# Kernel optimization log

Hardware: AMD Instinct MI355X
Metric: run time of the kernel (lower is better)

The kernel has to match this reference:

```python
import jax, jax.numpy as jnp
import numpy as np

N_GROUP = 64
GROUP_SIZE = 64
INPUT_DIM = 2048
BATCH = 8192
N_MONTN = 512


def setup_inputs() -> dict:
    key = jax.random.key(0)
    k1, k2, k3, k4, k5 = jax.random.split(key, 5)
    x = jax.random.normal(k1, (BATCH, INPUT_DIM), dtype=jnp.float32)
    weight = jax.random.normal(k2, (N_GROUP * GROUP_SIZE, INPUT_DIM), dtype=jnp.float32) * 0.02
    bias = jax.random.normal(k3, (N_GROUP * GROUP_SIZE,), dtype=jnp.float32) * 0.02
    rand_u = jax.random.uniform(k4, (BATCH,), dtype=jnp.float32)
    montn_index = jax.random.randint(k5, (N_MONTN,), 0, INPUT_DIM, dtype=jnp.int32)
    return {"x": x, "weight": weight, "bias": bias, "rand_u": rand_u,
            "montn_index": montn_index}


def reference(x, weight, bias, rand_u, montn_index):
    # Square the weights on monotone input columns (in-place in torch).
    w = weight.at[:, montn_index].set(weight[:, montn_index] ** 2)
    # y = x @ w^T + b  -> [B, n_group * n_group_size]
    y = jnp.einsum('bi,oi->bo', x, w) + bias
    B = y.shape[0]
    # per-group min over contiguous slices, then max over groups
    group_mins = y.reshape(B, N_GROUP, GROUP_SIZE).min(axis=2)  # [B, n_group]
    out = group_mins.max(axis=1)                                 # [B]
    # vectorized Bernoulli: 1.0 if u < sigmoid(out) else 0.0
    sample = (rand_u < jax.nn.sigmoid(out)).astype(jnp.float32)
    return sample.reshape(-1, 1)
```

## Files before the change

### kernel.cpp

```cpp
#include <hip/hip_runtime.h>
#include <cmath>


typedef _Float16 f16x8 __attribute__((ext_vector_type(8)));
typedef float f32x16 __attribute__((ext_vector_type(16)));

#define MARGIN_EPS 4e-3f
#define MAX_UNDEC 96

__device__ __forceinline__ void async_load16(const void* gptr, void* lptr) {
  __builtin_amdgcn_global_load_lds(
      (const __attribute__((address_space(1))) void*)gptr,
      (__attribute__((address_space(3))) void*)lptr, 16, 0, 0);
}

__device__ __forceinline__ float us2f(unsigned short u) {
  return (float)__builtin_bit_cast(_Float16, u);
}

__global__ void convert_split(float* __restrict__ x, float* __restrict__ wgt,
                              const int* __restrict__ montn,
                              int* __restrict__ count) {
  __shared__ unsigned msk[64];
  const int t = threadIdx.x, l = t & 63, w = t >> 6;
  const int r = blockIdx.x * 4 + w;
  const int use_mask = (r >= 8192) ? 1 : 0;
  if (blockIdx.x == 0 && t == 0) *count = 0;
  if (use_mask) {
    if (t < 64) msk[t] = 0u;
    __syncthreads();
    for (int j = t; j < 512; j += 256) {
      const int c = montn[j];
      atomicOr(&msk[c >> 5], 1u << (c & 31));
    }
    __syncthreads();
  }
  float* rowp = use_mask ? (wgt + (size_t)(r - 8192) * 2048)
                         : (x + (size_t)r * 2048);
  float4 v[8];
#pragma unroll
  for (int j = 0; j < 8; ++j) v[j] = ((const float4*)rowp)[l + 64 * j];
  unsigned mw[8];
#pragma unroll
  for (int j = 0; j < 8; ++j)
    mw[j] = use_mask ? msk[(l >> 3) + 8 * j] : 0u;

  unsigned short* up = (unsigned short*)rowp;
#pragma unroll
  for (int j = 0; j < 8; ++j) {
    unsigned short hs[4], ls[4];
    const float* fv = (const float*)&v[j];
#pragma unroll
    for (int c = 0; c < 4; ++c) {
      float f = fv[c];
      if ((mw[j] >> (4 * (l & 7) + c)) & 1u) f = f * f;
      _Float16 h = (_Float16)f;
      float res = f - (float)h;
      _Float16 lo = (_Float16)res;
      hs[c] = __builtin_bit_cast(unsigned short, h);
      ls[c] = __builtin_bit_cast(unsigned short, lo);
    }
    uint2 H, L;
    H.x = (unsigned)hs[0] | ((unsigned)hs[1] << 16);
    H.y = (unsigned)hs[2] | ((unsigned)hs[3] << 16);
    L.x = (unsigned)ls[0] | ((unsigned)ls[1] << 16);
    L.y = (unsigned)ls[2] | ((unsigned)ls[3] << 16);
    *((uint2*)(up + 4 * l + 256 * j)) = H;
    *((uint2*)(up + 2048 + 4 * l + 256 * j)) = L;
  }
}

__global__ __launch_bounds__(256, 4) void gemm_minmax(
    const unsigned short* __restrict__ X, const unsigned short* __restrict__ W,
    const float* __restrict__ bias, float* __restrict__ gmins) {
  __shared__ unsigned short As[128 * 64];
  __shared__ unsigned short Bs[128 * 64];
  const int t = threadIdx.x;
  const int lane = t & 63;
  const int w = t >> 6;
  const int wm = w >> 1, wn = w & 1;
  const int lin = blockIdx.x;
  const int sid = lin >> 3;
  const int m0 = (sid >> 2) * 128;
  const int n0 = ((lin & 7) * 4 + (sid & 3)) * 128;

  const int rowBase = w * 8 + (lane >> 3);
  const int gchunk = ((lane & 7) ^ ((lane >> 3) & 7)) * 8;
  size_t sA[4], sB[4];
#pragma unroll
  for (int c = 0; c < 4; ++c) {
    sA[c] = (size_t)(m0 + c * 32 + rowBase) * 4096 + gchunk;
    sB[c] = (size_t)(n0 + c * 32 + rowBase) * 4096 + gchunk;
  }
  unsigned short* ldsA[4];
  unsigned short* ldsB[4];
#pragma unroll
  for (int c = 0; c < 4; ++c) {
    ldsA[c] = As + c * 2048 + w * 512;
    ldsB[c] = Bs + c * 2048 + w * 512;
  }

  const int l31 = lane & 31, hi32 = lane >> 5;
  int arow[2], brow[2], swz[4];
#pragma unroll
  for (int i = 0; i < 2; ++i) {
    arow[i] = (wm * 64 + i * 32 + l31) * 64;
    brow[i] = (wn * 64 + i * 32 + l31) * 64;
  }
#pragma unroll
  for (int s = 0; s < 4; ++s) swz[s] = ((2 * s + hi32) ^ (lane & 7)) * 8;

  f32x16 acc[2][2];
#pragma unroll
  for (int i = 0; i < 2; ++i)
#pragma unroll
    for (int j = 0; j < 2; ++j) acc[i][j] = (f32x16)(0.f);

#pragma unroll 1
  for (int it = 0; it < 32; ++it) {
    const int kin = it * 64;
    __syncthreads();
#pragma unroll
    for (int c = 0; c < 4; ++c) {
      async_load16(X + sA[c] + kin, ldsA[c]);
      async_load16(W + sB[c] + kin, ldsB[c]);
    }
    __syncthreads();

#pragma unroll
    for (int s = 0; s < 4; ++s) {
      f16x8 a0 = *(const f16x8*)(As + arow[0] + swz[s]);
      f16x8 a1 = *(const f16x8*)(As + arow[1] + swz[s]);
      f16x8 b0 = *(const f16x8*)(Bs + brow[0] + swz[s]);
      f16x8 b1 = *(const f16x8*)(Bs + brow[1] + swz[s]);
      acc[0][0] = __builtin_amdgcn_mfma_f32_32x32x16_f16(a0, b0, acc[0][0], 0, 0, 0);
      acc[0][1] = __builtin_amdgcn_mfma_f32_32x32x16_f16(a0, b1, acc[0][1], 0, 0, 0);
      acc[1][0] = __builtin_amdgcn_mfma_f32_32x32x16_f16(a1, b0, acc[1][0], 0, 0, 0);
      acc[1][1] = __builtin_amdgcn_mfma_f32_32x32x16_f16(a1, b1, acc[1][1], 0, 0, 0);
    }
  }

  float bia[2];
#pragma unroll
  for (int nt = 0; nt < 2; ++nt) bia[nt] = bias[n0 + wn * 64 + nt * 32 + l31];
  const int grp = (n0 >> 6) + wn;
#pragma unroll
  for (int mt = 0; mt < 2; ++mt) {
#pragma unroll
    for (int r = 0; r < 16; ++r) {
      float v = fminf(acc[mt][0][r] + bia[0], acc[mt][1][r] + bia[1]);
      v = fminf(v, __shfl_xor(v, 1, 64));
      v = fminf(v, __shfl_xor(v, 2, 64));
      v = fminf(v, __shfl_xor(v, 4, 64));
      v = fminf(v, __shfl_xor(v, 8, 64));
      v = fminf(v, __shfl_xor(v, 16, 64));
      if (l31 == 0) {
        const int row = m0 + wm * 64 + mt * 32 + (r & 3) + 8 * (r >> 2) + 4 * hi32;
        gmins[(size_t)row * 64 + grp] = v;
      }
    }
  }
}

__global__ void finalize_margin(const float* __restrict__ gmins,
                                const float* __restrict__ rand_u,
                                float* __restrict__ out,
                                int* __restrict__ count, int* __restrict__ undec,
                                float4* __restrict__ ybuf4) {
  if (blockIdx.x < 384)
    ybuf4[(size_t)blockIdx.x * 256 + threadIdx.x] = (float4){0.f, 0.f, 0.f, 0.f};
  const int wv = threadIdx.x >> 6, lane = threadIdx.x & 63;
  const int row = blockIdx.x * 4 + wv;
  float v = gmins[(size_t)row * 64 + lane];
  v = fmaxf(v, __shfl_xor(v, 1, 64));
  v = fmaxf(v, __shfl_xor(v, 2, 64));
  v = fmaxf(v, __shfl_xor(v, 4, 64));
  v = fmaxf(v, __shfl_xor(v, 8, 64));
  v = fmaxf(v, __shfl_xor(v, 16, 64));
  v = fmaxf(v, __shfl_xor(v, 32, 64));
  if (lane == 0) {
    const float u = rand_u[row];
    const float slo = 1.0f / (1.0f + expf(-(v - MARGIN_EPS)));
    const float shi = 1.0f / (1.0f + expf(-(v + MARGIN_EPS)));
    if (u < slo) {
      out[row] = 1.0f;
    } else if (u >= shi) {
      out[row] = 0.0f;
    } else {
      const int i = atomicAdd(count, 1);
      if (i < 8192) undec[i] = row;
    }
  }
}

__global__ __launch_bounds__(256) void recompute_rows(
    const unsigned short* __restrict__ X, const unsigned short* __restrict__ W,
    const int* __restrict__ count, const int* __restrict__ undec,
    float* __restrict__ ybuf) {
  __shared__ float wf[64 * 129];
  __shared__ float part[256];
  const int g = blockIdx.x, kc = blockIdx.y;
  const int t = threadIdx.x;
  int n = *count;
  if (n > MAX_UNDEC) n = MAX_UNDEC;
  if (n == 0) return;

  {
    const int cl = t >> 2, ks = t & 3;
    const unsigned short* wp =
        W + (size_t)(g * 64 + cl) * 4096 + kc * 128 + ks * 32;
    float* dst = wf + cl * 129 + ks * 32;
#pragma unroll
    for (int i = 0; i < 32; i += 8) {
      uint4 hv = *(const uint4*)(wp + i);
      uint4 lv = *(const uint4*)(wp + 2048 + i);
      const unsigned* hw = (const unsigned*)&hv;
      const unsigned* lw = (const unsigned*)&lv;
#pragma unroll
      for (int m = 0; m < 4; ++m) {
        dst[i + 2 * m] = us2f((unsigned short)(hw[m] & 0xFFFF)) +
                         us2f((unsigned short)(lw[m] & 0xFFFF));
        dst[i + 2 * m + 1] = us2f((unsigned short)(hw[m] >> 16)) +
                             us2f((unsigned short)(lw[m] >> 16));
      }
    }
  }
  __syncthreads();

  const int col = t & 63, kq = t >> 6;
  const float* wcol = wf + col * 129 + kq * 32;
  for (int s = 0; s < n; ++s) {
    const int row = undec[s];
    const unsigned short* xp = X + (size_t)row * 4096 + kc * 128 + kq * 32;
    float acc = 0.f;
#pragma unroll
    for (int i = 0; i < 32; i += 8) {
      uint4 hv = *(const uint4*)(xp + i);
      uint4 lv = *(const uint4*)(xp + 2048 + i);
      const unsigned* hw = (const unsigned*)&hv;
      const unsigned* lw = (const unsigned*)&lv;
#pragma unroll
      for (int m = 0; m < 4; ++m) {
        const float x0 = us2f((unsigned short)(hw[m] & 0xFFFF)) +
                         us2f((unsigned short)(lw[m] & 0xFFFF));
        const float x1 = us2f((unsigned short)(hw[m] >> 16)) +
                         us2f((unsigned short)(lw[m] >> 16));
        acc = fmaf(x0, wcol[i + 2 * m], acc);
        acc = fmaf(x1, wcol[i + 2 * m + 1], acc);
      }
    }
    part[t] = acc;
    __syncthreads();
    if (t < 64) {
      const float y = part[t] + part[t + 64] + part[t + 128] + part[t + 192];
      atomicAdd(ybuf + (size_t)s * 4096 + g * 64 + t, y);
    }
    __syncthreads();
  }
}

__global__ void decide(const float* __restrict__ ybuf,
                       const int* __restrict__ undec, const int* __restrict__ count,
                       const float* __restrict__ bias,
                       const float* __restrict__ rand_u, float* __restrict__ out) {
  __shared__ float gm[64];
  int n = *count;
  if (n > MAX_UNDEC) n = MAX_UNDEC;
  const int s = blockIdx.x;
  if (s >= n) return;
  const int t = threadIdx.x;
  const int g = t >> 2, p4 = t & 3;
  const float* yb = ybuf + (size_t)s * 4096;
  const int c0 = g * 64 + p4 * 16;
  float m = 3.4e38f;
#pragma unroll
  for (int e = 0; e < 16; ++e) m = fminf(m, yb[c0 + e] + bias[c0 + e]);
  m = fminf(m, __shfl_xor(m, 1, 64));
  m = fminf(m, __shfl_xor(m, 2, 64));
  if (p4 == 0) gm[g] = m;
  __syncthreads();
  if (t < 64) {
    float v = gm[t];
    v = fmaxf(v, __shfl_xor(v, 1, 64));
    v = fmaxf(v, __shfl_xor(v, 2, 64));
    v = fmaxf(v, __shfl_xor(v, 4, 64));
    v = fmaxf(v, __shfl_xor(v, 8, 64));
    v = fmaxf(v, __shfl_xor(v, 16, 64));
    v = fmaxf(v, __shfl_xor(v, 32, 64));
    if (t == 0) {
      const int row = undec[s];
      const float sg = 1.0f / (1.0f + expf(-v));
      out[row] = (rand_u[row] < sg) ? 1.0f : 0.0f;
    }
  }
}

extern "C" void kernel_launch(void* const* d_in, const int* in_sizes, int n_in,
                              void* d_out, int out_size, void* d_ws, size_t ws_size,
                              hipStream_t stream) {
  float* x = (float*)d_in[0];
  float* weight = (float*)d_in[1];
  const float* bias = (const float*)d_in[2];
  const float* rand_u = (const float*)d_in[3];
  const int* montn = (const int*)d_in[4];
  float* out = (float*)d_out;

  char* ws = (char*)d_ws;
  int* count = (int*)ws;
  int* undec = (int*)(ws + 256);
  float* ybuf = (float*)(ws + 65536);
  float* gmins = (float*)(ws + 65536 + 1572864);

  convert_split<<<3072, 256, 0, stream>>>(x, weight, montn, count);
  gemm_minmax<<<2048, 256, 0, stream>>>(
      (const unsigned short*)x, (const unsigned short*)weight, bias, gmins);
  finalize_margin<<<2048, 256, 0, stream>>>(gmins, rand_u, out, count, undec,
                                            (float4*)ybuf);
  recompute_rows<<<dim3(64, 16), 256, 0, stream>>>(
      (const unsigned short*)x, (const unsigned short*)weight, count, undec, ybuf);
  decide<<<MAX_UNDEC, 256, 0, stream>>>(ybuf, undec, count, bias, rand_u, out);
}
```

Baseline: 328.0 us.

## Double-buffer LDS tiles and switch GEMM to 16x16x32 MFMA fragments

The main GEMM loop now uses double-buffered LDS with a K-step of 32, so the async global-to-LDS load of the next tile is issued before computing on the current one. This removes one barrier per iteration and lets load latency overlap the MFMAs. The wave tile is recomputed with 4x4 16x16x32 MFMAs instead of 2x2 32x32x16, and the swizzle and min-reduction epilogue are adjusted to match. The trade-off is twice as many loop iterations with smaller tiles, and a different accumulator register layout.

```diff
diff --git a/kernel.cpp b/kernel.cpp
--- a/kernel.cpp
+++ b/kernel.cpp
@@ -3,7 +3,7 @@
 
 
 typedef _Float16 f16x8 __attribute__((ext_vector_type(8)));
-typedef float f32x16 __attribute__((ext_vector_type(16)));
+typedef float f32x4 __attribute__((ext_vector_type(4)));
 
 #define MARGIN_EPS 4e-3f
 #define MAX_UNDEC 96
@@ -73,8 +73,8 @@
 __global__ __launch_bounds__(256, 4) void gemm_minmax(
     const unsigned short* __restrict__ X, const unsigned short* __restrict__ W,
     const float* __restrict__ bias, float* __restrict__ gmins) {
-  __shared__ unsigned short As[128 * 64];
-  __shared__ unsigned short Bs[128 * 64];
+  __shared__ unsigned short As[2 * 128 * 32];
+  __shared__ unsigned short Bs[2 * 128 * 32];
   const int t = threadIdx.x;
   const int lane = t & 63;
   const int w = t >> 6;
@@ -84,78 +84,81 @@
   const int m0 = (sid >> 2) * 128;
   const int n0 = ((lin & 7) * 4 + (sid & 3)) * 128;
 
-  const int rowBase = w * 8 + (lane >> 3);
-  const int gchunk = ((lane & 7) ^ ((lane >> 3) & 7)) * 8;
-  size_t sA[4], sB[4];
-#pragma unroll
-  for (int c = 0; c < 4; ++c) {
-    sA[c] = (size_t)(m0 + c * 32 + rowBase) * 4096 + gchunk;
-    sB[c] = (size_t)(n0 + c * 32 + rowBase) * 4096 + gchunk;
-  }
-  unsigned short* ldsA[4];
-  unsigned short* ldsB[4];
-#pragma unroll
-  for (int c = 0; c < 4; ++c) {
-    ldsA[c] = As + c * 2048 + w * 512;
-    ldsB[c] = Bs + c * 2048 + w * 512;
-  }
-
-  const int l31 = lane & 31, hi32 = lane >> 5;
-  int arow[2], brow[2], swz[4];
-#pragma unroll
-  for (int i = 0; i < 2; ++i) {
-    arow[i] = (wm * 64 + i * 32 + l31) * 64;
-    brow[i] = (wn * 64 + i * 32 + l31) * 64;
-  }
-#pragma unroll
-  for (int s = 0; s < 4; ++s) swz[s] = ((2 * s + hi32) ^ (lane & 7)) * 8;
-
-  f32x16 acc[2][2];
-#pragma unroll
-  for (int i = 0; i < 2; ++i)
-#pragma unroll
-    for (int j = 0; j < 2; ++j) acc[i][j] = (f32x16)(0.f);
+  const int rowS = w * 16 + (lane >> 2);
+  const int gch = (((lane & 3) ^ ((lane >> 2) & 3)) * 8);
+  size_t sA[2], sB[2];
+#pragma unroll
+  for (int c = 0; c < 2; ++c) {
+    sA[c] = (size_t)(m0 + c * 64 + rowS) * 4096 + gch;
+    sB[c] = (size_t)(n0 + c * 64 + rowS) * 4096 + gch;
+  }
+
+  const int am = lane & 15, quad = lane >> 4;
+  int aoff[4], boff[4];
+#pragma unroll
+  for (int i = 0; i < 4; ++i) {
+    const int ar = wm * 64 + i * 16 + am;
+    const int br = wn * 64 + i * 16 + am;
+    aoff[i] = ar * 32 + ((quad ^ (am & 3)) * 8);
+    boff[i] = br * 32 + ((quad ^ (am & 3)) * 8);
+  }
+
+  f32x4 acc[4][4];
+#pragma unroll
+  for (int i = 0; i < 4; ++i)
+#pragma unroll
+    for (int j = 0; j < 4; ++j) acc[i][j] = (f32x4){0.f, 0.f, 0.f, 0.f};
+
+#pragma unroll
+  for (int c = 0; c < 2; ++c) {
+    async_load16(X + sA[c], As + c * 2048 + w * 512);
+    async_load16(W + sB[c], Bs + c * 2048 + w * 512);
+  }
 
 #pragma unroll 1
-  for (int it = 0; it < 32; ++it) {
-    const int kin = it * 64;
-    __syncthreads();
-#pragma unroll
-    for (int c = 0; c < 4; ++c) {
-      async_load16(X + sA[c] + kin, ldsA[c]);
-      async_load16(W + sB[c] + kin, ldsB[c]);
-    }
-    __syncthreads();
-
-#pragma unroll
-    for (int s = 0; s < 4; ++s) {
-      f16x8 a0 = *(const f16x8*)(As + arow[0] + swz[s]);
-      f16x8 a1 = *(const f16x8*)(As + arow[1] + swz[s]);
-      f16x8 b0 = *(const f16x8*)(Bs + brow[0] + swz[s]);
-      f16x8 b1 = *(const f16x8*)(Bs + brow[1] + swz[s]);
-      acc[0][0] = __builtin_amdgcn_mfma_f32_32x32x16_f16(a0, b0, acc[0][0], 0, 0, 0);
-      acc[0][1] = __builtin_amdgcn_mfma_f32_32x32x16_f16(a0, b1, acc[0][1], 0, 0, 0);
-      acc[1][0] = __builtin_amdgcn_mfma_f32_32x32x16_f16(a1, b0, acc[1][0], 0, 0, 0);
-      acc[1][1] = __builtin_amdgcn_mfma_f32_32x32x16_f16(a1, b1, acc[1][1], 0, 0, 0);
-    }
-  }
-
-  float bia[2];
-#pragma unroll
-  for (int nt = 0; nt < 2; ++nt) bia[nt] = bias[n0 + wn * 64 + nt * 32 + l31];
+  for (int it = 0; it < 64; ++it) {
+    const int buf = it & 1;
+    __syncthreads();
+    if (it + 1 < 64) {
+      const int kin = (it + 1) * 32;
+      const int ob = (buf ^ 1) * 4096;
+#pragma unroll
+      for (int c = 0; c < 2; ++c) {
+        async_load16(X + sA[c] + kin, As + ob + c * 2048 + w * 512);
+        async_load16(W + sB[c] + kin, Bs + ob + c * 2048 + w * 512);
+      }
+    }
+    const unsigned short* Ab = As + buf * 4096;
+    const unsigned short* Bb = Bs + buf * 4096;
+    f16x8 av[4], bv[4];
+#pragma unroll
+    for (int i = 0; i < 4; ++i) av[i] = *(const f16x8*)(Ab + aoff[i]);
+#pragma unroll
+    for (int i = 0; i < 4; ++i) bv[i] = *(const f16x8*)(Bb + boff[i]);
+#pragma unroll
+    for (int mb = 0; mb < 4; ++mb)
+#pragma unroll
+      for (int nb = 0; nb < 4; ++nb)
+        acc[mb][nb] = __builtin_amdgcn_mfma_f32_16x16x32_f16(
+            av[mb], bv[nb], acc[mb][nb], 0, 0, 0);
+  }
+
+  float bv4[4];
+#pragma unroll
+  for (int nb = 0; nb < 4; ++nb) bv4[nb] = bias[n0 + wn * 64 + nb * 16 + am];
   const int grp = (n0 >> 6) + wn;
 #pragma unroll
-  for (int mt = 0; mt < 2; ++mt) {
-#pragma unroll
-    for (int r = 0; r < 16; ++r) {
-      float v = fminf(acc[mt][0][r] + bia[0], acc[mt][1][r] + bia[1]);
+  for (int mb = 0; mb < 4; ++mb) {
+#pragma unroll
+    for (int reg = 0; reg < 4; ++reg) {
+      float v = fminf(fminf(acc[mb][0][reg] + bv4[0], acc[mb][1][reg] + bv4[1]),
+                      fminf(acc[mb][2][reg] + bv4[2], acc[mb][3][reg] + bv4[3]));
       v = fminf(v, __shfl_xor(v, 1, 64));
       v = fminf(v, __shfl_xor(v, 2, 64));
       v = fminf(v, __shfl_xor(v, 4, 64));
       v = fminf(v, __shfl_xor(v, 8, 64));
-      v = fminf(v, __shfl_xor(v, 16, 64));
-      if (l31 == 0) {
-        const int row = m0 + wm * 64 + mt * 32 + (r & 3) + 8 * (r >> 2) + 4 * hi32;
+      if (am == 0) {
+        const int row = m0 + wm * 64 + mb * 16 + quad * 4 + reg;
         gmins[(size_t)row * 64 + grp] = v;
       }
     }
```

After: 321.9 us. Within noise of the previous version (-1.9%).
